# Kernel optimization log

Measured on AMD Instinct MI355X. Metric: run time of the kernel, lower is better.

## Reference

```python
import jax, jax.numpy as jnp
import numpy as np

N, FEAT, HID, D_ATT, N_CLS, TXT = 50000, 2048, 1024, 512, 2, 768


def _lin(key, fan_in, fan_out):
    k1, k2 = jax.random.split(key)
    s = 1.0 / np.sqrt(fan_in)
    W = jax.random.uniform(k1, (fan_in, fan_out), jnp.float32, -s, s)
    b = jax.random.uniform(k2, (fan_out,), jnp.float32, -s, s)
    return W, b


def setup_inputs() -> dict:
    key = jax.random.key(0)
    ks = jax.random.split(key, 9)
    x = jax.random.normal(ks[0], (N, FEAT), jnp.float32)
    text_emb = jax.random.normal(ks[1], (1, TXT), jnp.float32)
    W1, b1 = _lin(ks[2], FEAT, HID)
    Wa, ba = _lin(ks[3], HID, D_ATT)
    Wb, bb = _lin(ks[4], HID, D_ATT)
    Wc, bc = _lin(ks[5], D_ATT, 1)
    Wt, bt = _lin(ks[6], TXT, HID)
    Wcls, bcls = _lin(ks[7], HID, N_CLS)
    return {"x": x, "text_emb": text_emb, "W1": W1, "b1": b1,
            "Wa": Wa, "ba": ba, "Wb": Wb, "bb": bb, "Wc": Wc, "bc": bc,
            "Wt": Wt, "bt": bt, "Wcls": Wcls, "bcls": bcls}


def reference(x, text_emb, W1, b1, Wa, ba, Wb, bb, Wc, bc, Wt, bt, Wcls, bcls):
    # attention_net: Linear(2048->1024) + ReLU (dropout is identity in eval)
    h = jax.nn.relu(x @ W1 + b1)                      # [N, 1024]
    # Attn_Net_Gated: tanh branch * sigmoid branch -> Linear(512->1)
    a = jnp.tanh(h @ Wa + ba)                         # [N, 512]
    g = jax.nn.sigmoid(h @ Wb + bb)                   # [N, 512]
    A = (a * g) @ Wc + bc                             # [N, 1]
    A = jax.nn.softmax(A.T, axis=1)                   # [1, N] attention over instances
    M = A @ h                                         # [1, 1024] pooled slide embedding
    # text_to_vision: Linear(768->1024) + ReLU (dropout identity in eval)
    t = jax.nn.relu(text_emb @ Wt + bt)               # [1, 1024]
    M = M + t
    logits = M @ Wcls + bcls                          # [1, 2]
    return logits
```

## Files before the change

kernel.cpp:

```cpp
#include <hip/hip_runtime.h>
#include <cstdint>
#include <cstddef>

#define DEV __device__ __forceinline__

typedef unsigned short u16;
typedef unsigned int   u32;
typedef __attribute__((ext_vector_type(8))) short bf16x8;
typedef __attribute__((ext_vector_type(4))) float f32x4;

static constexpr int NROWS = 50000;
static constexpr int FEAT  = 2048;
static constexpr int HID   = 1024;
static constexpr int DATT  = 512;
static constexpr int TXTD  = 768;

DEV u32 bfbits(float f) {
  u32 u = __float_as_uint(f);
  return (u + 0x7fffu + ((u >> 16) & 1u)) >> 16;
}
DEV u32 pk2(float lo, float hi) { return bfbits(lo) | (bfbits(hi) << 16); }
DEV float bflo(u32 u) { return __uint_as_float(u << 16); }
DEV float bfhi(u32 u) { return __uint_as_float(u & 0xffff0000u); }

DEV void gld_lds16(const u16* g, u16* l) {
  __builtin_amdgcn_global_load_lds(
      (const __attribute__((address_space(1))) unsigned int*)g,
      (__attribute__((address_space(3))) unsigned int*)l, 16, 0, 0);
}

__global__ void k_t_w1(const float* __restrict__ W, u16* __restrict__ out) {
  __shared__ float tile[64][65];
  const int KT = FEAT / 64;
  int bid = blockIdx.x;
  int kt = bid % KT, nt = bid / KT;
  int k0 = kt * 64, n0 = nt * 64;
  int t = threadIdx.x;
#pragma unroll
  for (int i = 0; i < 16; i++) {
    int idx = t + i * 256;
    int kk = idx >> 6, nn = idx & 63;
    tile[kk][nn] = W[(size_t)(k0 + kk) * HID + n0 + nn];
  }
  __syncthreads();
#pragma unroll
  for (int i = 0; i < 16; i++) {
    int idx = t + i * 256;
    int nn = idx >> 6, kk = idx & 63;
    out[(size_t)(n0 + nn) * FEAT + k0 + kk] = (u16)bfbits(tile[kk][nn]);
  }
}

__global__ void k_t_wab(const float* __restrict__ Wa, const float* __restrict__ Wb,
                        u16* __restrict__ out) {
  __shared__ float tile[64][65];
  const int KT = HID / 64;
  int bid = blockIdx.x;
  int kt = bid % KT, nt = bid / KT;
  int k0 = kt * 64, n0 = nt * 64;
  int t = threadIdx.x;
#pragma unroll
  for (int i = 0; i < 16; i++) {
    int idx = t + i * 256;
    int kk = idx >> 6, nn = idx & 63;
    int n = n0 + nn;
    const float* src = (n & 1) ? Wb : Wa;
    tile[kk][nn] = src[(size_t)(k0 + kk) * DATT + (n >> 1)];
  }
  __syncthreads();
#pragma unroll
  for (int i = 0; i < 16; i++) {
    int idx = t + i * 256;
    int nn = idx >> 6, kk = idx & 63;
    out[(size_t)(n0 + nn) * HID + k0 + kk] = (u16)bfbits(tile[kk][nn]);
  }
}

DEV void tile_mfma(const char* bufA, const char* bufB, f32x4 acc[4][4],
                   int lo, int hi, int wr, int wc) {
#pragma unroll
  for (int ks = 0; ks < 2; ks++) {
    bf16x8 av[4], bv[4];
#pragma unroll
    for (int m = 0; m < 4; m++) {
      int row = wr * 64 + m * 16 + lo;
      int off = (row * 128 + ks * 64 + hi * 16) ^ ((row & 7) << 4);
      av[m] = *(const bf16x8*)(bufA + off);
    }
#pragma unroll
    for (int n = 0; n < 4; n++) {
      int col = wc * 64 + n * 16 + lo;
      int off = (col * 128 + ks * 64 + hi * 16) ^ ((col & 7) << 4);
      bv[n] = *(const bf16x8*)(bufB + off);
    }
#pragma unroll
    for (int m = 0; m < 4; m++)
#pragma unroll
      for (int n = 0; n < 4; n++)
        acc[m][n] = __builtin_amdgcn_mfma_f32_16x16x32_bf16(av[m], bv[n], acc[m][n], 0, 0, 0);
  }
}

__global__ __launch_bounds__(256, 2) void k_gemm1(const float* __restrict__ X,
                                                  const u16* __restrict__ BT,
                                                  const float* __restrict__ b1,
                                                  u16* __restrict__ Hb) {
  __shared__ __align__(16) char smem[2][32768];
  int t = threadIdx.x;
  int l = t & 63, w = t >> 6;
  int lo = l & 15, hi = l >> 4;
  int wr = w >> 1, wc = w & 1;

  int nwg = gridDim.x, bid = blockIdx.x;
  int li = ((nwg & 7) == 0) ? ((bid & 7) * (nwg >> 3) + (bid >> 3)) : bid;
  int mt = li >> 3, nt = li & 7;
  int rowbase = mt * 128, ncb0 = nt * 128;

  f32x4 acc[4][4];
#pragma unroll
  for (int m = 0; m < 4; m++)
#pragma unroll
    for (int n = 0; n < 4; n++) acc[m][n] = {0.f, 0.f, 0.f, 0.f};

  const int KT = FEAT / 64;

  auto stageB = [&](int kt_, int buf) {
    int kbase = kt_ * 64;
    char* bufB = smem[buf] + 16384;
#pragma unroll
    for (int i = 0; i < 4; i++) {
      int s = t + i * 256;
      int nn = s >> 3, k8 = (s & 7) ^ (nn & 7);
      const u16* src = BT + (size_t)(ncb0 + nn) * FEAT + kbase + k8 * 8;
      u16* dst = (u16*)(bufB + i * 4096 + w * 1024);
      gld_lds16(src, dst);
    }
  };
  auto stageA = [&](int kt_, int buf) {
    int kbase = kt_ * 64;
    char* bufA = smem[buf];
#pragma unroll
    for (int i = 0; i < 4; i++) {
      int s = t + i * 256;
      int row = s >> 3, k8 = s & 7;
      int grow = rowbase + row; if (grow >= NROWS) grow = NROWS - 1;
      const float4* src = (const float4*)(X + (size_t)grow * FEAT + kbase + k8 * 8);
      float4 f0 = src[0], f1 = src[1];
      uint4 v; v.x = pk2(f0.x, f0.y); v.y = pk2(f0.z, f0.w);
      v.z = pk2(f1.x, f1.y); v.w = pk2(f1.z, f1.w);
      int off = (row * 128 + k8 * 16) ^ ((row & 7) << 4);
      *(uint4*)(bufA + off) = v;
    }
  };

  stageB(0, 0);
  stageA(0, 0);
  __syncthreads();
  for (int kt_ = 0; kt_ < KT - 1; ++kt_) {
    int nb = (kt_ + 1) & 1;
    stageB(kt_ + 1, nb);
    stageA(kt_ + 1, nb);
    tile_mfma(smem[kt_ & 1], smem[kt_ & 1] + 16384, acc, lo, hi, wr, wc);
    __syncthreads();
  }
  tile_mfma(smem[(KT - 1) & 1], smem[(KT - 1) & 1] + 16384, acc, lo, hi, wr, wc);

  int mrow0 = rowbase + wr * 64;
  int ncol0 = ncb0 + wc * 64;
#pragma unroll
  for (int n = 0; n < 4; n++) {
    int col = ncol0 + n * 16 + lo;
    float bias = b1[col];
#pragma unroll
    for (int m = 0; m < 4; m++)
#pragma unroll
      for (int i = 0; i < 4; i++) {
        int row = mrow0 + m * 16 + hi * 4 + i;
        if (row < NROWS) {
          float v = acc[m][n][i] + bias;
          v = fmaxf(v, 0.f);
          Hb[(size_t)row * HID + col] = (u16)bfbits(v);
        }
      }
  }
}

__global__ __launch_bounds__(256, 2) void k_gemm2(const u16* __restrict__ Hb,
                                                  const u16* __restrict__ BT,
                                                  const float* __restrict__ ba,
                                                  const float* __restrict__ bb,
                                                  const float* __restrict__ Wc,
                                                  float* __restrict__ scores) {
  __shared__ __align__(16) char smem[2][32768];
  int t = threadIdx.x;
  int l = t & 63, w = t >> 6;
  int lo = l & 15, hi = l >> 4;
  int wr = w >> 1, wc_ = w & 1;

  int nwg = gridDim.x, bid = blockIdx.x;
  int li = ((nwg & 7) == 0) ? ((bid & 7) * (nwg >> 3) + (bid >> 3)) : bid;
  int mt = li >> 3, nt = li & 7;
  int rowbase = mt * 128, ncb0 = nt * 128;

  f32x4 acc[4][4];
#pragma unroll
  for (int m = 0; m < 4; m++)
#pragma unroll
    for (int n = 0; n < 4; n++) acc[m][n] = {0.f, 0.f, 0.f, 0.f};

  const int KT = HID / 64;

  auto stage = [&](int kt_, int buf) {
    int kbase = kt_ * 64;
    char* bufA = smem[buf];
    char* bufB = smem[buf] + 16384;
#pragma unroll
    for (int i = 0; i < 4; i++) {
      int s = t + i * 256;
      int nn = s >> 3, k8 = (s & 7) ^ (nn & 7);
      int grow = rowbase + nn; if (grow >= NROWS) grow = NROWS - 1;
      gld_lds16(Hb + (size_t)grow * HID + kbase + k8 * 8,
                (u16*)(bufA + i * 4096 + w * 1024));
      gld_lds16(BT + (size_t)(ncb0 + nn) * HID + kbase + k8 * 8,
                (u16*)(bufB + i * 4096 + w * 1024));
    }
  };

  stage(0, 0);
  __syncthreads();
  for (int kt_ = 0; kt_ < KT - 1; ++kt_) {
    stage(kt_ + 1, (kt_ + 1) & 1);
    tile_mfma(smem[kt_ & 1], smem[kt_ & 1] + 16384, acc, lo, hi, wr, wc_);
    __syncthreads();
  }
  tile_mfma(smem[(KT - 1) & 1], smem[(KT - 1) & 1] + 16384, acc, lo, hi, wr, wc_);

  int mrow0 = rowbase + wr * 64;
  int ncol0 = ncb0 + wc_ * 64;
  float rs[4][4];
#pragma unroll
  for (int m = 0; m < 4; m++)
#pragma unroll
    for (int i = 0; i < 4; i++) rs[m][i] = 0.f;

#pragma unroll
  for (int n = 0; n < 4; n++) {
    int col = ncol0 + n * 16 + lo;
    int j = col >> 1;
    bool odd = (col & 1);
    float bias = odd ? bb[j] : ba[j];
    float wcj = Wc[j];
    float scl  = odd ? 0.5f : 1.0f;
    float pmul = odd ? 0.5f : 1.0f;
    float padd = odd ? 0.5f : 0.0f;
#pragma unroll
    for (int m = 0; m < 4; m++)
#pragma unroll
      for (int i = 0; i < 4; i++) {
        float v = acc[m][n][i] + bias;
        float act = fmaf(tanhf(v * scl), pmul, padd);
        float prt = __shfl_xor(act, 1);
        rs[m][i] = fmaf(act * prt, wcj, rs[m][i]);
      }
  }
#pragma unroll
  for (int m = 0; m < 4; m++)
#pragma unroll
    for (int i = 0; i < 4; i++) {
      float sv = rs[m][i];
      sv += __shfl_xor(sv, 2);
      sv += __shfl_xor(sv, 4);
      sv += __shfl_xor(sv, 8);
      if (lo == 0) {
        int row = mrow0 + m * 16 + hi * 4 + i;
        if (row < NROWS) atomicAdd(&scores[row], sv);
      }
    }
}

__global__ void k_red1(const float* __restrict__ s, int n, float2* __restrict__ part) {
  __shared__ float sm[256];
  int t = threadIdx.x;
  int stride = gridDim.x * 256;
  float m = -3.4e38f;
  for (int i = blockIdx.x * 256 + t; i < n; i += stride) m = fmaxf(m, s[i]);
  sm[t] = m; __syncthreads();
  for (int st = 128; st; st >>= 1) { if (t < st) sm[t] = fmaxf(sm[t], sm[t + st]); __syncthreads(); }
  float bm = sm[0];
  __syncthreads();
  float se = 0.f;
  for (int i = blockIdx.x * 256 + t; i < n; i += stride) se += expf(s[i] - bm);
  sm[t] = se; __syncthreads();
  for (int st = 128; st; st >>= 1) { if (t < st) sm[t] += sm[t + st]; __syncthreads(); }
  if (t == 0) part[blockIdx.x] = make_float2(bm, sm[0]);
}

__global__ void k_red2(const float2* __restrict__ part, float* __restrict__ red2) {
  int t = threadIdx.x;
  float2 p = part[t];
  float m = p.x;
#pragma unroll
  for (int off = 32; off; off >>= 1) m = fmaxf(m, __shfl_down(m, off));
  m = __shfl(m, 0);
  float se = p.y * expf(p.x - m);
#pragma unroll
  for (int off = 32; off; off >>= 1) se += __shfl_down(se, off);
  if (t == 0) { red2[0] = m; red2[1] = se; }
}

__global__ void k_pool(const u16* __restrict__ Hb, const float* __restrict__ scores,
                       const float* __restrict__ red2, float* __restrict__ Mpool) {
  int t = threadIdx.x;
  int c = t * 4;
  float gmax = red2[0];
  float ginv = 1.0f / red2[1];
  float a0 = 0, a1 = 0, a2 = 0, a3 = 0;
  int r0 = blockIdx.x * 128;
  int rend = r0 + 128; if (rend > NROWS) rend = NROWS;
  for (int r = r0; r < rend; ++r) {
    float wgt = expf(scores[r] - gmax) * ginv;
    uint2 hv = *(const uint2*)(Hb + (size_t)r * HID + c);
    a0 = fmaf(wgt, bflo(hv.x), a0);
    a1 = fmaf(wgt, bfhi(hv.x), a1);
    a2 = fmaf(wgt, bflo(hv.y), a2);
    a3 = fmaf(wgt, bfhi(hv.y), a3);
  }
  atomicAdd(&Mpool[c + 0], a0);
  atomicAdd(&Mpool[c + 1], a1);
  atomicAdd(&Mpool[c + 2], a2);
  atomicAdd(&Mpool[c + 3], a3);
}

__global__ void k_final(const float* __restrict__ Mpool, const float* __restrict__ text,
                        const float* __restrict__ Wt, const float* __restrict__ bt,
                        const float* __restrict__ Wcls, const float* __restrict__ bcls,
                        float* __restrict__ out) {
  __shared__ float Mv[HID];
  __shared__ float red0[256], red1[256];
  int t = threadIdx.x;
#pragma unroll
  for (int rep = 0; rep < 4; rep++) {
    int n = t + rep * 256;
    float accv = bt[n];
    for (int k = 0; k < TXTD; k++) accv = fmaf(text[k], Wt[(size_t)k * HID + n], accv);
    accv = fmaxf(accv, 0.f);
    Mv[n] = Mpool[n] + accv;
  }
  __syncthreads();
  float p0 = 0.f, p1 = 0.f;
#pragma unroll
  for (int rep = 0; rep < 4; rep++) {
    int n = t + rep * 256;
    p0 = fmaf(Mv[n], Wcls[n * 2 + 0], p0);
    p1 = fmaf(Mv[n], Wcls[n * 2 + 1], p1);
  }
  red0[t] = p0; red1[t] = p1;
  __syncthreads();
  for (int st = 128; st; st >>= 1) {
    if (t < st) { red0[t] += red0[t + st]; red1[t] += red1[t + st]; }
    __syncthreads();
  }
  if (t == 0) { out[0] = red0[0] + bcls[0]; out[1] = red1[0] + bcls[1]; }
}

extern "C" void kernel_launch(void* const* d_in, const int* in_sizes, int n_in,
                              void* d_out, int out_size, void* d_ws, size_t ws_size,
                              hipStream_t stream) {
  const float* x    = (const float*)d_in[0];
  const float* text = (const float*)d_in[1];
  const float* W1   = (const float*)d_in[2];
  const float* b1   = (const float*)d_in[3];
  const float* Wa   = (const float*)d_in[4];
  const float* ba   = (const float*)d_in[5];
  const float* Wb   = (const float*)d_in[6];
  const float* bb   = (const float*)d_in[7];
  const float* Wc   = (const float*)d_in[8];
  const float* Wt   = (const float*)d_in[10];
  const float* bt   = (const float*)d_in[11];
  const float* Wcls = (const float*)d_in[12];
  const float* bcls = (const float*)d_in[13];

  const size_t off_w1t = 0;
  const size_t off_wg  = 4194304;
  const size_t off_hb  = 6291456;
  const size_t off_sc  = 108691456;
  const size_t off_pt  = 108891456;
  const size_t off_r2  = 108891968;
  const size_t off_m   = 108892032;
  const size_t NEED    = 108896128;
  if (ws_size < NEED) return;

  char* ws = (char*)d_ws;
  u16*   W1T    = (u16*)(ws + off_w1t);
  u16*   WgT    = (u16*)(ws + off_wg);
  u16*   Hb     = (u16*)(ws + off_hb);
  float* scores = (float*)(ws + off_sc);
  float2* part  = (float2*)(ws + off_pt);
  float* red2   = (float*)(ws + off_r2);
  float* Mpool  = (float*)(ws + off_m);

  hipMemsetAsync(scores, 0, NROWS * sizeof(float), stream);
  hipMemsetAsync(Mpool, 0, HID * sizeof(float), stream);

  k_t_w1 <<<(FEAT / 64) * (HID / 64), 256, 0, stream>>>(W1, W1T);
  k_t_wab<<<(HID / 64) * (HID / 64),  256, 0, stream>>>(Wa, Wb, WgT);

  const int MT = (NROWS + 127) / 128;
  k_gemm1<<<MT * 8, 256, 0, stream>>>(x, W1T, b1, Hb);
  k_gemm2<<<MT * 8, 256, 0, stream>>>(Hb, WgT, ba, bb, Wc, scores);

  k_red1<<<64, 256, 0, stream>>>(scores, NROWS, part);
  k_red2<<<1, 64, 0, stream>>>(part, red2);
  k_pool<<<MT, 256, 0, stream>>>(Hb, scores, red2, Mpool);
  k_final<<<1, 256, 0, stream>>>(Mpool, text, Wt, bt, Wcls, bcls, (float*)d_out);
}
```

Measured before the change: 1.318 ms.

## Single-buffer LDS in both GEMMs to raise occupancy, precompute staging addresses

Both GEMM kernels drop the LDS double buffer (64KB to 32KB) and raise launch bounds from 2 to 4 blocks per CU. The goal is to hide global-load latency through more resident workgroups instead of in-block prefetch. Per-thread global and LDS staging addresses are now computed once before the K loop. The main loop becomes compute, sync, load, sync, which serializes loads and MFMA inside a block and adds a barrier per K step. The tighter register budget at 4 blocks per CU may also cause spills.

```diff
diff --git a/kernel.cpp b/kernel.cpp
--- a/kernel.cpp
+++ b/kernel.cpp
@@ -101,11 +101,11 @@
   }
 }
 
-__global__ __launch_bounds__(256, 2) void k_gemm1(const float* __restrict__ X,
+__global__ __launch_bounds__(256, 4) void k_gemm1(const float* __restrict__ X,
                                                   const u16* __restrict__ BT,
                                                   const float* __restrict__ b1,
                                                   u16* __restrict__ Hb) {
-  __shared__ __align__(16) char smem[2][32768];
+  __shared__ __align__(16) char smem[32768];
   int t = threadIdx.x;
   int l = t & 63, w = t >> 6;
   int lo = l & 15, hi = l >> 4;
@@ -124,46 +124,49 @@
 
   const int KT = FEAT / 64;
 
-  auto stageB = [&](int kt_, int buf) {
+  int r0 = t >> 3;
+  int k8a = t & 7;
+  int swzA = (r0 & 7) << 4;
+  int k8b = (t & 7) ^ (r0 & 7);
+  const float* pA[4];
+  const u16*   pB[4];
+  int offA[4];
+  u16* dstB[4];
+#pragma unroll
+  for (int i = 0; i < 4; i++) {
+    int row = r0 + i * 32;
+    int grow = rowbase + row; if (grow >= NROWS) grow = NROWS - 1;
+    pA[i] = X + (size_t)grow * FEAT + k8a * 8;
+    offA[i] = (row * 128 + k8a * 16) ^ swzA;
+    pB[i] = BT + (size_t)(ncb0 + row) * FEAT + k8b * 8;
+    dstB[i] = (u16*)(smem + 16384 + i * 4096 + w * 1024);
+  }
+
+  auto stage = [&](int kt_) {
     int kbase = kt_ * 64;
-    char* bufB = smem[buf] + 16384;
+#pragma unroll
+    for (int i = 0; i < 4; i++)
+      gld_lds16(pB[i] + kbase, dstB[i]);
 #pragma unroll
     for (int i = 0; i < 4; i++) {
-      int s = t + i * 256;
-      int nn = s >> 3, k8 = (s & 7) ^ (nn & 7);
-      const u16* src = BT + (size_t)(ncb0 + nn) * FEAT + kbase + k8 * 8;
-      u16* dst = (u16*)(bufB + i * 4096 + w * 1024);
-      gld_lds16(src, dst);
-    }
-  };
-  auto stageA = [&](int kt_, int buf) {
-    int kbase = kt_ * 64;
-    char* bufA = smem[buf];
-#pragma unroll
-    for (int i = 0; i < 4; i++) {
-      int s = t + i * 256;
-      int row = s >> 3, k8 = s & 7;
-      int grow = rowbase + row; if (grow >= NROWS) grow = NROWS - 1;
-      const float4* src = (const float4*)(X + (size_t)grow * FEAT + kbase + k8 * 8);
+      const float4* src = (const float4*)(pA[i] + kbase);
       float4 f0 = src[0], f1 = src[1];
       uint4 v; v.x = pk2(f0.x, f0.y); v.y = pk2(f0.z, f0.w);
       v.z = pk2(f1.x, f1.y); v.w = pk2(f1.z, f1.w);
-      int off = (row * 128 + k8 * 16) ^ ((row & 7) << 4);
-      *(uint4*)(bufA + off) = v;
+      *(uint4*)(smem + offA[i]) = v;
     }
   };
 
-  stageB(0, 0);
-  stageA(0, 0);
-  __syncthreads();
-  for (int kt_ = 0; kt_ < KT - 1; ++kt_) {
-    int nb = (kt_ + 1) & 1;
-    stageB(kt_ + 1, nb);
-    stageA(kt_ + 1, nb);
-    tile_mfma(smem[kt_ & 1], smem[kt_ & 1] + 16384, acc, lo, hi, wr, wc);
+  stage(0);
+  __syncthreads();
+  for (int kt_ = 0; kt_ < KT; ++kt_) {
+    tile_mfma(smem, smem + 16384, acc, lo, hi, wr, wc);
     __syncthreads();
-  }
-  tile_mfma(smem[(KT - 1) & 1], smem[(KT - 1) & 1] + 16384, acc, lo, hi, wr, wc);
+    if (kt_ + 1 < KT) {
+      stage(kt_ + 1);
+      __syncthreads();
+    }
+  }
 
   int mrow0 = rowbase + wr * 64;
   int ncol0 = ncb0 + wc * 64;
@@ -185,13 +188,13 @@
   }
 }
 
-__global__ __launch_bounds__(256, 2) void k_gemm2(const u16* __restrict__ Hb,
+__global__ __launch_bounds__(256, 4) void k_gemm2(const u16* __restrict__ Hb,
                                                   const u16* __restrict__ BT,
                                                   const float* __restrict__ ba,
                                                   const float* __restrict__ bb,
                                                   const float* __restrict__ Wc,
                                                   float* __restrict__ scores) {
-  __shared__ __align__(16) char smem[2][32768];
+  __shared__ __align__(16) char smem[32768];
   int t = threadIdx.x;
   int l = t & 63, w = t >> 6;
   int lo = l & 15, hi = l >> 4;
@@ -210,30 +213,41 @@
 
   const int KT = HID / 64;
 
-  auto stage = [&](int kt_, int buf) {
+  int r0 = t >> 3;
+  int k8 = (t & 7) ^ (r0 & 7);
+  const u16* pA[4];
+  const u16* pB[4];
+  u16* dstA[4];
+  u16* dstB[4];
+#pragma unroll
+  for (int i = 0; i < 4; i++) {
+    int row = r0 + i * 32;
+    int grow = rowbase + row; if (grow >= NROWS) grow = NROWS - 1;
+    pA[i] = Hb + (size_t)grow * HID + k8 * 8;
+    pB[i] = BT + (size_t)(ncb0 + row) * HID + k8 * 8;
+    dstA[i] = (u16*)(smem + i * 4096 + w * 1024);
+    dstB[i] = (u16*)(smem + 16384 + i * 4096 + w * 1024);
+  }
+
+  auto stage = [&](int kt_) {
     int kbase = kt_ * 64;
-    char* bufA = smem[buf];
-    char* bufB = smem[buf] + 16384;
 #pragma unroll
     for (int i = 0; i < 4; i++) {
-      int s = t + i * 256;
-      int nn = s >> 3, k8 = (s & 7) ^ (nn & 7);
-      int grow = rowbase + nn; if (grow >= NROWS) grow = NROWS - 1;
-      gld_lds16(Hb + (size_t)grow * HID + kbase + k8 * 8,
-                (u16*)(bufA + i * 4096 + w * 1024));
-      gld_lds16(BT + (size_t)(ncb0 + nn) * HID + kbase + k8 * 8,
-                (u16*)(bufB + i * 4096 + w * 1024));
+      gld_lds16(pA[i] + kbase, dstA[i]);
+      gld_lds16(pB[i] + kbase, dstB[i]);
     }
   };
 
-  stage(0, 0);
-  __syncthreads();
-  for (int kt_ = 0; kt_ < KT - 1; ++kt_) {
-    stage(kt_ + 1, (kt_ + 1) & 1);
-    tile_mfma(smem[kt_ & 1], smem[kt_ & 1] + 16384, acc, lo, hi, wr, wc_);
+  stage(0);
+  __syncthreads();
+  for (int kt_ = 0; kt_ < KT; ++kt_) {
+    tile_mfma(smem, smem + 16384, acc, lo, hi, wr, wc_);
     __syncthreads();
-  }
-  tile_mfma(smem[(KT - 1) & 1], smem[(KT - 1) & 1] + 16384, acc, lo, hi, wr, wc_);
+    if (kt_ + 1 < KT) {
+      stage(kt_ + 1);
+      __syncthreads();
+    }
+  }
 
   int mrow0 = rowbase + wr * 64;
   int ncol0 = ncb0 + wc_ * 64;
```

Measured after the change: 1.612 ms. +22.3%, slower.
